# Optimization experiments

Measured on AMD Instinct MI355X. Metric: run time of the kernel, lower is better.

The kernel has to match this reference:

```python
import jax, jax.numpy as jnp
import numpy as np
import math

N_HEAD = 8
LN_EPS = 1e-5


def _layernorm(x, g, b):
    mu = jnp.mean(x, axis=-1, keepdims=True)
    var = jnp.mean(jnp.square(x - mu), axis=-1, keepdims=True)
    return (x - mu) / jnp.sqrt(var + LN_EPS) * g + b


def setup_inputs() -> dict:
    key0 = jax.random.key(0)
    ks = jax.random.split(key0, 12)
    B, L, D, E = 4, 512, 256, 5  # batch, agents, n_embd, edge_feats_dim

    def w(k, shape):
        return jax.random.normal(k, shape, dtype=jnp.float32) * 0.02

    return {
        "key": jax.random.normal(ks[0], (B, L, D), jnp.float32),
        "value": jax.random.normal(ks[1], (B, L, D), jnp.float32),
        "query": jax.random.normal(ks[2], (B, L, D), jnp.float32),
        "atten_masks": jax.random.randint(ks[3], (B, L, L), 0, 2).astype(jnp.int32),
        "edge_feats": jax.random.normal(ks[4], (B, L, L, E), jnp.float32),
        # Linear weights stored [in, out] so forward is x @ W + b
        "Wk": w(ks[5], (D, D)), "bk": jnp.zeros((D,), jnp.float32),
        "Wq": w(ks[6], (D, D)), "bq": jnp.zeros((D,), jnp.float32),
        "Wv": w(ks[7], (D, D)), "bv": jnp.zeros((D,), jnp.float32),
        "Wp": w(ks[8], (D, D)), "bp": jnp.zeros((D,), jnp.float32),
        "We1": w(ks[9], (E, D)), "be1": jnp.zeros((D,), jnp.float32),
        "ln_g": jnp.ones((D,), jnp.float32), "ln_b": jnp.zeros((D,), jnp.float32),
        "We2": w(ks[10], (D, N_HEAD)), "be2": jnp.zeros((N_HEAD,), jnp.float32),
    }


def reference(key, value, query, atten_masks, edge_feats,
              Wk, bk, Wq, bq, Wv, bv, Wp, bp,
              We1, be1, ln_g, ln_b, We2, be2):
    B, L, D = query.shape
    hd = D // N_HEAD
    # QKV projections -> [B, H, L, hd]
    q = (query @ Wq + bq).reshape(B, L, N_HEAD, hd).transpose(0, 2, 1, 3)
    k = (key @ Wk + bk).reshape(B, L, N_HEAD, hd).transpose(0, 2, 1, 3)
    v = (value @ Wv + bv).reshape(B, L, N_HEAD, hd).transpose(0, 2, 1, 3)
    # scaled attention scores [B, H, L, L]
    att = jnp.einsum('bhqd,bhkd->bhqk', q, k) * (1.0 / math.sqrt(hd))
    # edge-feature additive bias: Linear -> ReLU -> LayerNorm -> Linear(per-head)
    e = jax.nn.relu(edge_feats @ We1 + be1)          # [B, L, L, D]
    e = _layernorm(e, ln_g, ln_b)
    e = e @ We2 + be2                                # [B, L, L, H]
    att = att + e.transpose(0, 3, 1, 2)
    # additive mask (0 -> -inf), softmax over keys
    att = jnp.where(atten_masks[:, None, :, :] == 0, -jnp.inf, att)
    att = jax.nn.softmax(att, axis=-1)
    y = jnp.einsum('bhqk,bhkd->bhqd', att, v)        # [B, H, L, hd]
    y = y.transpose(0, 2, 1, 3).reshape(B, L, D)
    return y @ Wp + bp
```

## Files before the change

kernel.cpp:

```cpp
#include <hip/hip_runtime.h>
#include <hip/hip_bf16.h>

#define L_SEQ 512
#define D_EMB 256
#define NH 8
#define HD 32
#define LL (L_SEQ * L_SEQ)

typedef __attribute__((ext_vector_type(8))) short short8;
typedef __attribute__((ext_vector_type(4))) float f32x4;
typedef unsigned short ushort;

__device__ __forceinline__ float bf2f(ushort u) {
    unsigned int x = ((unsigned int)u) << 16;
    float f;
    __builtin_memcpy(&f, &x, 4);
    return f;
}
__device__ __forceinline__ ushort f2bf(float x) {
    __hip_bfloat16 h = __float2bfloat16(x);
    ushort u;
    __builtin_memcpy(&u, &h, 2);
    return u;
}
__device__ __forceinline__ unsigned int fbits(float x) {
    unsigned int u;
    __builtin_memcpy(&u, &x, 4);
    return u;
}
__device__ __forceinline__ float asf(unsigned int u) {
    float f;
    __builtin_memcpy(&f, &u, 4);
    return f;
}
__device__ __forceinline__ unsigned int cvt_pk_bf16(float a, float b) {
    unsigned int r;
    asm("v_cvt_pk_bf16_f32 %0, %1, %2" : "=v"(r) : "v"(a), "v"(b));
    return r;
}
__device__ __forceinline__ unsigned int packhi(unsigned int y, unsigned int x) {
    return __builtin_amdgcn_perm(y, x, 0x07060302u);
}
__device__ __forceinline__ uint2 cvt_hilo2(float v0, float v1) {
    unsigned int hi = cvt_pk_bf16(v0, v1);
    float h0 = asf(hi << 16);
    float h1 = asf(hi & 0xffff0000u);
    unsigned int lo = cvt_pk_bf16(v0 - h0, v1 - h1);
    uint2 r; r.x = hi; r.y = lo;
    return r;
}
__device__ __forceinline__ void gload_lds16(const float* g, float* l) {
    __builtin_amdgcn_global_load_lds(
        (const __attribute__((address_space(1))) void*)g,
        (__attribute__((address_space(3))) void*)l, 16, 0, 0);
}

__global__ __launch_bounds__(256) void prep_kernel(
    const float* __restrict__ We1, const float* __restrict__ be1,
    const float* __restrict__ g,   const float* __restrict__ bta,
    const float* __restrict__ We2, const float* __restrict__ be2,
    const float* __restrict__ Wq, const float* __restrict__ Wk,
    const float* __restrict__ Wv, const float* __restrict__ Wp,
    ushort* __restrict__ W1G, ushort* __restrict__ B2G, float* __restrict__ tail,
    ushort* __restrict__ WThi, ushort* __restrict__ WTlo)
{
    int t = threadIdx.x;
    if (blockIdx.x != 0) {
        int bx = blockIdx.x - 1;
        int w = bx >> 4, ny = bx & 15;
        const float* W = (w == 0) ? Wq : (w == 1) ? Wk : (w == 2) ? Wv : Wp;
        ushort* dh = WThi + (size_t)w * 65536;
        ushort* dl = WTlo + (size_t)w * 65536;
        int n = ny * 16 + (t >> 4);
        int k0 = (t & 15) * 16;
        ushort hbuf[16], lbuf[16];
#pragma unroll
        for (int kk = 0; kk < 16; ++kk) {
            float v = W[(size_t)(k0 + kk) * 256 + n];
            unsigned int hb = fbits(v) + 0x8000u;
            ushort hi = (ushort)(hb >> 16);
            float res = v - bf2f(hi);
            hbuf[kk] = hi;
            lbuf[kk] = (ushort)((fbits(res) + 0x8000u) >> 16);
        }
        *(short8*)(dh + (size_t)n * 256 + k0)     = *(short8*)&hbuf[0];
        *(short8*)(dh + (size_t)n * 256 + k0 + 8) = *(short8*)&hbuf[8];
        *(short8*)(dl + (size_t)n * 256 + k0)     = *(short8*)&lbuf[0];
        *(short8*)(dl + (size_t)n * 256 + k0 + 8) = *(short8*)&lbuf[8];
        return;
    }

    __shared__ float red[16][256];
    float gd = g[t], bd = bta[t];
#pragma unroll
    for (int h = 0; h < 8; ++h) {
        float w2 = We2[t * 8 + h];
        red[h][t] = gd * w2;
        red[8 + h][t] = bd * w2;
    }
    __syncthreads();
    for (int off = 128; off > 0; off >>= 1) {
        if (t < off) {
#pragma unroll
            for (int row = 0; row < 16; ++row) red[row][t] += red[row][t + off];
        }
        __syncthreads();
    }
    if (t < 8) {
        tail[t] = red[t][0];
        tail[8 + t] = red[8 + t][0] + be2[t];
    }
    if (t >= 16 && t < 32) tail[t] = 0.f;

    for (int idx = t; idx < 8192; idx += 256) {
        int j = idx & 7, lane = (idx >> 3) & 63, tile = idx >> 9;
        int m = lane & 15, q = lane >> 4;
        int k = q * 8 + j;
        int d = (m >> 2) * 64 + tile * 4 + (m & 3);
        float v = 0.f;
        bool lo = false;
        if (k < 5)        v = We1[k * 256 + d];
        else if (k < 10)  { v = We1[(k - 5) * 256 + d]; lo = true; }
        else if (k < 15)  v = We1[(k - 10) * 256 + d];
        else if (k == 15) v = be1[d];
        else if (k == 16) { v = be1[d]; lo = true; }
        ushort hi = f2bf(v);
        W1G[idx] = lo ? f2bf(v - bf2f(hi)) : hi;
    }
    for (int idx = t; idx < 4096; idx += 256) {
        int j = idx & 7, lane = (idx >> 3) & 63, kc = idx >> 9;
        int n = lane & 15, q = lane >> 4;
        int d = q * 64 + kc * 8 + j;
        ushort out;
        if (n < 8)       out = f2bf(g[d] * We2[d * 8 + n]);
        else if (n == 8) out = 0x3F80;
        else             out = 0;
        B2G[idx] = out;
    }
}

__device__ __forceinline__ void gemm_body(
    const float* __restrict__ A, const ushort* __restrict__ BH,
    const ushort* __restrict__ BL, const float* __restrict__ bias,
    float* __restrict__ C, float* __restrict__ Ct,
    int bx, int by, char* smem)
{
    ushort* Ahi = (ushort*)smem;
    ushort* Alo = (ushort*)(smem + 5120);

    int tid = threadIdx.x;
    int wv = tid >> 6, lane = tid & 63;
    int m = lane & 15, quad = lane >> 4;
    int bm = bx * 64, bn = by * 64;

    int sm = tid >> 2, sg = (tid & 3) * 8;
    const float* Arow = A + (size_t)(bm + sm) * 256 + sg;

    int nrow = bn + wv * 16 + m;
    const ushort* bhp = BH + (size_t)nrow * 256 + quad * 8;
    const ushort* blp = BL + (size_t)nrow * 256 + quad * 8;

    f32x4 acc[4];
#pragma unroll
    for (int mt = 0; mt < 4; ++mt) acc[mt] = (f32x4){0.f, 0.f, 0.f, 0.f};

    for (int k0 = 0; k0 < 256; k0 += 32) {
        float4 a0 = *(const float4*)(Arow + k0);
        float4 a1 = *(const float4*)(Arow + k0 + 4);
        uint2 c0 = cvt_hilo2(a0.x, a0.y);
        uint2 c1 = cvt_hilo2(a0.z, a0.w);
        uint2 c2 = cvt_hilo2(a1.x, a1.y);
        uint2 c3 = cvt_hilo2(a1.z, a1.w);
        if (k0) __syncthreads();
        uint4 hq; hq.x = c0.x; hq.y = c1.x; hq.z = c2.x; hq.w = c3.x;
        uint4 lq; lq.x = c0.y; lq.y = c1.y; lq.z = c2.y; lq.w = c3.y;
        *(uint4*)&Ahi[sm * 40 + sg] = hq;
        *(uint4*)&Alo[sm * 40 + sg] = lq;
        __syncthreads();

        short8 bhi = *(const short8*)(bhp + k0);
        short8 blo = *(const short8*)(blp + k0);
#pragma unroll
        for (int mt = 0; mt < 4; ++mt) {
            short8 ahi = *(const short8*)&Ahi[(mt * 16 + m) * 40 + quad * 8];
            short8 alo = *(const short8*)&Alo[(mt * 16 + m) * 40 + quad * 8];
            acc[mt] = __builtin_amdgcn_mfma_f32_16x16x32_bf16(ahi, blo, acc[mt], 0, 0, 0);
            acc[mt] = __builtin_amdgcn_mfma_f32_16x16x32_bf16(alo, bhi, acc[mt], 0, 0, 0);
            acc[mt] = __builtin_amdgcn_mfma_f32_16x16x32_bf16(ahi, bhi, acc[mt], 0, 0, 0);
        }
    }

    float bn_bias = bias[nrow];
    if (Ct) {
        int bb = bm >> 9, l0 = bm & 511;
        float* outp = Ct + ((size_t)(bb * 256 + nrow)) * 512 + l0 + quad * 4;
#pragma unroll
        for (int mt = 0; mt < 4; ++mt) {
            float4 o;
            o.x = acc[mt][0] + bn_bias; o.y = acc[mt][1] + bn_bias;
            o.z = acc[mt][2] + bn_bias; o.w = acc[mt][3] + bn_bias;
            *(float4*)(outp + mt * 16) = o;
        }
    } else {
#pragma unroll
        for (int mt = 0; mt < 4; ++mt) {
#pragma unroll
            for (int r = 0; r < 4; ++r) {
                C[(size_t)(bm + mt * 16 + quad * 4 + r) * 256 + nrow] = acc[mt][r] + bn_bias;
            }
        }
    }
}

__device__ __forceinline__ short8 make_ef8(const float4& evA, float evB, int q) {
    unsigned int hb0 = fbits(evA.x), hb1 = fbits(evA.y), hb2 = fbits(evA.z),
                 hb3 = fbits(evA.w), hb4 = fbits(evB);
    float e0 = evA.x - asf(hb0 & 0xffff0000u);
    float e1 = evA.y - asf(hb1 & 0xffff0000u);
    float e2 = evA.z - asf(hb2 & 0xffff0000u);
    float e3 = evA.w - asf(hb3 & 0xffff0000u);
    float e4 = evB   - asf(hb4 & 0xffff0000u);
    unsigned int la0 = fbits(e0) + 0x8000u;
    unsigned int la1 = fbits(e1) + 0x8000u;
    unsigned int la2 = fbits(e2) + 0x8000u;
    unsigned int la3 = fbits(e3) + 0x8000u;
    unsigned int la4 = fbits(e4) + 0x8000u;
    unsigned int A0v = packhi(hb1, hb0);
    unsigned int A1v = packhi(hb3, hb2);
    unsigned int A2v = packhi(hb0, hb4);
    unsigned int A3v = packhi(hb2, hb1);
    unsigned int B0v = packhi(hb4, hb3);
    unsigned int B1v = packhi(la1, la0);
    unsigned int B2v = packhi(la3, la2);
    unsigned int B3v = packhi(0x3F800000u, la4);
    uint4 efd;
    bool isq0 = (q == 0), isq1 = (q == 1), isq2 = (q == 2);
    efd.x = isq0 ? A0v : isq1 ? B0v : isq2 ? 0x3F80u : 0u;
    efd.y = isq0 ? A1v : isq1 ? B1v : 0u;
    efd.z = isq0 ? A2v : isq1 ? B2v : 0u;
    efd.w = isq0 ? A3v : isq1 ? B3v : 0u;
    short8 ef8;
    __builtin_memcpy(&ef8, &efd, 16);
    return ef8;
}

__device__ __forceinline__ void ln_store(
    const f32x4& acc, const f32x4& acc2, float shv, float bbv,
    int lane, int n, int q, ushort* __restrict__ E2,
    int b, int i, int jb)
{
    const float inv256 = 1.0f / 256.0f;
    int base = lane & 48;
    float er[4];
#pragma unroll
    for (int r = 0; r < 4; ++r) {
        float sm = __shfl(acc[r], base + 8);
        float sq = __shfl(acc2[r], base + (base >> 2) + r);
        float dot = acc[r];
        float mu = sm * inv256;
        float var = fmaf(-mu, mu, sq * inv256);
        float rs = rsqrtf(var + 1e-5f);
        er[r] = fmaf(dot - mu * shv, rs, bbv);
    }
    if (n < 8) {
        uint2 outv;
        outv.x = cvt_pk_bf16(er[0], er[1]);
        outv.y = cvt_pk_bf16(er[2], er[3]);
        size_t basep = (((size_t)(b * NH + n) * L_SEQ + i) * L_SEQ) + jb + q * 4;
        *(uint2*)(E2 + basep) = outv;
    }
}

__device__ __forceinline__ void edge_body(
    const float* __restrict__ EF, const ushort* __restrict__ W1G,
    const ushort* __restrict__ B2G, const float* __restrict__ tail,
    ushort* __restrict__ E2, int bi, char* smem)
{
    int tid = threadIdx.x;
    {
        const uint4* s1 = (const uint4*)W1G;
        uint4* d1 = (uint4*)smem;
#pragma unroll
        for (int k = 0; k < 4; ++k) d1[tid + k * 256] = s1[tid + k * 256];
    }
    int wv = tid >> 6, lane = tid & 63;
    int q = lane >> 4, n = lane & 15;

    short8 b2f[8];
#pragma unroll
    for (int kc = 0; kc < 8; ++kc)
        b2f[kc] = *(const short8*)(B2G + (kc * 64 + lane) * 8);

    int b = bi >> 9, i = bi & 511;
    size_t rowbase = (size_t)bi * 512;

    float shv = tail[n];
    float bbv = tail[8 + n];

    const float* efbase = EF + rowbase * 5;
    int pair0 = wv * 32 + n;

    const float* p0 = efbase + (size_t)pair0 * 5;
    float4 evA0 = *(const float4*)p0;        float evB0 = p0[4];
    float4 evA1 = *(const float4*)(p0 + 80); float evB1 = p0[84];

    __syncthreads();
    const short8* w1l = (const short8*)smem;

    const f32x4 z = {0.f, 0.f, 0.f, 0.f};

    for (int iter = 0; iter < 4; ++iter) {
        float4 nA0, nA1; float nB0 = 0.f, nB1 = 0.f;
        if (iter < 3) {
            const float* pn = efbase + (size_t)((iter + 1) * 128 + pair0) * 5;
            nA0 = *(const float4*)pn;        nB0 = pn[4];
            nA1 = *(const float4*)(pn + 80); nB1 = pn[84];
        }
        int jb0 = iter * 128 + wv * 32;

        short8 ef0 = make_ef8(evA0, evB0, q);
        short8 ef1 = make_ef8(evA1, evB1, q);

        f32x4 acc0 = z, acc20 = z, acc1 = z, acc21 = z;
#pragma unroll
        for (int kc = 0; kc < 8; ++kc) {
            short8 wa = w1l[2 * kc * 64 + lane];
            short8 wb = w1l[(2 * kc + 1) * 64 + lane];
            short8 b2 = b2f[kc];
            f32x4 dA0 = __builtin_amdgcn_mfma_f32_16x16x32_bf16(wa, ef0, z, 0, 0, 0);
            f32x4 dB0 = __builtin_amdgcn_mfma_f32_16x16x32_bf16(wb, ef0, z, 0, 0, 0);
            f32x4 dA1 = __builtin_amdgcn_mfma_f32_16x16x32_bf16(wa, ef1, z, 0, 0, 0);
            f32x4 dB1 = __builtin_amdgcn_mfma_f32_16x16x32_bf16(wb, ef1, z, 0, 0, 0);
            uint4 av0, av1;
            av0.x = cvt_pk_bf16(fmaxf(dA0[0], 0.f), fmaxf(dA0[1], 0.f));
            av0.y = cvt_pk_bf16(fmaxf(dA0[2], 0.f), fmaxf(dA0[3], 0.f));
            av0.z = cvt_pk_bf16(fmaxf(dB0[0], 0.f), fmaxf(dB0[1], 0.f));
            av0.w = cvt_pk_bf16(fmaxf(dB0[2], 0.f), fmaxf(dB0[3], 0.f));
            av1.x = cvt_pk_bf16(fmaxf(dA1[0], 0.f), fmaxf(dA1[1], 0.f));
            av1.y = cvt_pk_bf16(fmaxf(dA1[2], 0.f), fmaxf(dA1[3], 0.f));
            av1.z = cvt_pk_bf16(fmaxf(dB1[0], 0.f), fmaxf(dB1[1], 0.f));
            av1.w = cvt_pk_bf16(fmaxf(dB1[2], 0.f), fmaxf(dB1[3], 0.f));
            short8 a0, a1;
            __builtin_memcpy(&a0, &av0, 16);
            __builtin_memcpy(&a1, &av1, 16);
            acc0  = __builtin_amdgcn_mfma_f32_16x16x32_bf16(a0, b2, acc0, 0, 0, 0);
            acc20 = __builtin_amdgcn_mfma_f32_16x16x32_bf16(a0, a0, acc20, 0, 0, 0);
            acc1  = __builtin_amdgcn_mfma_f32_16x16x32_bf16(a1, b2, acc1, 0, 0, 0);
            acc21 = __builtin_amdgcn_mfma_f32_16x16x32_bf16(a1, a1, acc21, 0, 0, 0);
        }

        ln_store(acc0, acc20, shv, bbv, lane, n, q, E2, b, i, jb0);
        ln_store(acc1, acc21, shv, bbv, lane, n, q, E2, b, i, jb0 + 16);

        evA0 = nA0; evB0 = nB0;
        evA1 = nA1; evB1 = nB1;
    }
}

__global__ __launch_bounds__(256, 4) void fused_qkv_edge(
    const float* __restrict__ query, const float* __restrict__ key,
    const float* __restrict__ value,
    const ushort* __restrict__ WThi, const ushort* __restrict__ WTlo,
    const float* __restrict__ bq, const float* __restrict__ bk,
    const float* __restrict__ bv,
    float* __restrict__ Qw, float* __restrict__ Ktw, float* __restrict__ Vw,
    const float* __restrict__ EF, const ushort* __restrict__ W1G,
    const ushort* __restrict__ B2G, const float* __restrict__ tail,
    ushort* __restrict__ E2)
{
    __shared__ __align__(16) char smem[16384];
    int bid = blockIdx.x;
    if (bid < 384) {
        int z = bid >> 7, rem = bid & 127;
        int bx = rem & 31, by = rem >> 5;
        if (z == 0)
            gemm_body(query, WThi + 0 * 65536, WTlo + 0 * 65536, bq, Qw, nullptr, bx, by, smem);
        else if (z == 1)
            gemm_body(key,   WThi + 1 * 65536, WTlo + 1 * 65536, bk, nullptr, Ktw, bx, by, smem);
        else
            gemm_body(value, WThi + 2 * 65536, WTlo + 2 * 65536, bv, Vw, nullptr, bx, by, smem);
    } else {
        edge_body(EF, W1G, B2G, tail, E2, bid - 384, smem);
    }
}

__global__ __launch_bounds__(256) void gemm_out(
    const float* __restrict__ A, const ushort* __restrict__ BH,
    const ushort* __restrict__ BL, const float* __restrict__ bias,
    float* __restrict__ C)
{
    __shared__ __align__(16) char smem[10240];
    gemm_body(A, BH, BL, bias, C, nullptr, blockIdx.x, blockIdx.y, smem);
}

__global__ __launch_bounds__(256, 4) void attn_kernel(
    const float* __restrict__ Q, const float* __restrict__ Kt,
    const float* __restrict__ V, const ushort* __restrict__ E2,
    const int* __restrict__ MSK, float* __restrict__ Y)
{
    __shared__ __align__(16) float stage[2][4096];
    __shared__ ushort pbuf[4][512][4];

    int bh = blockIdx.x;
    int b = bh >> 3, h = bh & 7;
    int tid = threadIdx.x;
    int wv = tid >> 6, lane = tid & 63;
    int i0 = blockIdx.y * 16;
    int i = i0 + wv * 4;

    const float* Ktb = Kt + (size_t)bh * (HD * L_SEQ);
    const float* Vb  = V + (size_t)b * L_SEQ * D_EMB + h * HD;

    int wvu = __builtin_amdgcn_readfirstlane(wv);
    const float* Qs = Q + ((size_t)(b * L_SEQ + i0 + wvu * 4)) * 256 + h * HD;

    size_t erow = ((size_t)bh * L_SEQ + i) * L_SEQ;
    size_t mrow = ((size_t)b * L_SEQ + i) * L_SEQ;

    unsigned int e2p[4][4];
    unsigned int mkb[4];
#pragma unroll
    for (int r = 0; r < 4; ++r) {
        unsigned int mb = 0;
#pragma unroll
        for (int c = 0; c < 4; ++c) {
            int j = c * 128 + 2 * lane;
            e2p[r][c] = *(const unsigned int*)(E2 + erow + (size_t)r * L_SEQ + j);
            int2 mv = *(const int2*)(MSK + mrow + (size_t)r * L_SEQ + j);
            mb |= (mv.x != 0 ? 1u : 0u) << (2 * c);
            mb |= (mv.y != 0 ? 1u : 0u) << (2 * c + 1);
        }
        mkb[r] = mb;
    }

    float s[4][8];
#pragma unroll
    for (int r = 0; r < 4; ++r)
#pragma unroll
        for (int t = 0; t < 8; ++t) s[r][t] = 0.f;

    int kd0 = tid >> 5, ksj = (tid & 31) * 4;
#pragma unroll
    for (int p = 0; p < 4; ++p)
        gload_lds16(Ktb + (size_t)(p * 8 + kd0) * L_SEQ + ksj,
                    &stage[0][(p * 8 + kd0) * 128 + ksj]);

    for (int c = 0; c < 4; ++c) {
        __syncthreads();
        if (c < 3) {
#pragma unroll
            for (int p = 0; p < 4; ++p)
                gload_lds16(Ktb + (size_t)(p * 8 + kd0) * L_SEQ + (c + 1) * 128 + ksj,
                            &stage[(c + 1) & 1][(p * 8 + kd0) * 128 + ksj]);
        }
        const float* stg = stage[c & 1];
        int c2 = c * 2;
#pragma unroll
        for (int d = 0; d < HD; ++d) {
            float q0 = Qs[0 * 256 + d];
            float q1 = Qs[1 * 256 + d];
            float q2 = Qs[2 * 256 + d];
            float q3 = Qs[3 * 256 + d];
            float2 kv = *(const float2*)&stg[d * 128 + 2 * lane];
            s[0][c2]     = fmaf(q0, kv.x, s[0][c2]);
            s[0][c2 + 1] = fmaf(q0, kv.y, s[0][c2 + 1]);
            s[1][c2]     = fmaf(q1, kv.x, s[1][c2]);
            s[1][c2 + 1] = fmaf(q1, kv.y, s[1][c2 + 1]);
            s[2][c2]     = fmaf(q2, kv.x, s[2][c2]);
            s[2][c2 + 1] = fmaf(q2, kv.y, s[2][c2 + 1]);
            s[3][c2]     = fmaf(q3, kv.x, s[3][c2]);
            s[3][c2 + 1] = fmaf(q3, kv.y, s[3][c2 + 1]);
        }
    }

    int vj0 = tid >> 3, vdd = (tid & 7) * 4;
#pragma unroll
    for (int p = 0; p < 4; ++p)
        gload_lds16(Vb + (size_t)(p * 32 + vj0) * D_EMB + vdd,
                    &stage[0][(p * 32 + vj0) * 32 + vdd]);

    const float scl = 0.17677669529663687f;
#pragma unroll
    for (int r = 0; r < 4; ++r) {
        float m = -3.0e38f;
#pragma unroll
        for (int idx = 0; idx < 8; ++idx) {
            int c = idx >> 1, u = idx & 1;
            unsigned int pk = e2p[r][c];
            float e = bf2f((ushort)(u ? (pk >> 16) : (pk & 0xffff)));
            int mk = (mkb[r] >> idx) & 1;
            float v = mk ? fmaf(s[r][idx], scl, e) : -1e30f;
            s[r][idx] = v;
            m = fmaxf(m, v);
        }
#pragma unroll
        for (int o = 32; o > 0; o >>= 1) m = fmaxf(m, __shfl_xor(m, o));
        float ssum = 0.f;
#pragma unroll
        for (int idx = 0; idx < 8; ++idx) {
            float p = __expf(s[r][idx] - m);
            s[r][idx] = p;
            ssum += p;
        }
#pragma unroll
        for (int o = 32; o > 0; o >>= 1) ssum += __shfl_xor(ssum, o);
        float inv = 1.0f / ssum;
#pragma unroll
        for (int idx = 0; idx < 8; ++idx) s[r][idx] *= inv;
    }
#pragma unroll
    for (int c = 0; c < 4; ++c) {
        int c2 = c * 2;
        uint4 w;
        w.x = cvt_pk_bf16(s[0][c2],     s[1][c2]);
        w.y = cvt_pk_bf16(s[2][c2],     s[3][c2]);
        w.z = cvt_pk_bf16(s[0][c2 + 1], s[1][c2 + 1]);
        w.w = cvt_pk_bf16(s[2][c2 + 1], s[3][c2 + 1]);
        *(uint4*)&pbuf[wv][c * 128 + 2 * lane][0] = w;
    }

    int dg = lane >> 3, js = lane & 7;
    float4 acc[4];
#pragma unroll
    for (int r = 0; r < 4; ++r) { acc[r].x = 0.f; acc[r].y = 0.f; acc[r].z = 0.f; acc[r].w = 0.f; }

    for (int c = 0; c < 4; ++c) {
        __syncthreads();
        if (c < 3) {
#pragma unroll
            for (int p = 0; p < 4; ++p)
                gload_lds16(Vb + (size_t)((c + 1) * 128 + p * 32 + vj0) * D_EMB + vdd,
                            &stage[(c + 1) & 1][(p * 32 + vj0) * 32 + vdd]);
        }
        const float* stg = stage[c & 1];
#pragma unroll
        for (int jb = 0; jb < 16; ++jb) {
            int jj = jb * 8 + js;
            float4 v4 = *(const float4*)&stg[jj * 32 + dg * 4];
            uint2 pu = *(const uint2*)&pbuf[wv][c * 128 + jj][0];
            float p0 = asf(pu.x << 16);
            float p1 = asf(pu.x & 0xffff0000u);
            float p2 = asf(pu.y << 16);
            float p3 = asf(pu.y & 0xffff0000u);
            acc[0].x = fmaf(p0, v4.x, acc[0].x);
            acc[0].y = fmaf(p0, v4.y, acc[0].y);
            acc[0].z = fmaf(p0, v4.z, acc[0].z);
            acc[0].w = fmaf(p0, v4.w, acc[0].w);
            acc[1].x = fmaf(p1, v4.x, acc[1].x);
            acc[1].y = fmaf(p1, v4.y, acc[1].y);
            acc[1].z = fmaf(p1, v4.z, acc[1].z);
            acc[1].w = fmaf(p1, v4.w, acc[1].w);
            acc[2].x = fmaf(p2, v4.x, acc[2].x);
            acc[2].y = fmaf(p2, v4.y, acc[2].y);
            acc[2].z = fmaf(p2, v4.z, acc[2].z);
            acc[2].w = fmaf(p2, v4.w, acc[2].w);
            acc[3].x = fmaf(p3, v4.x, acc[3].x);
            acc[3].y = fmaf(p3, v4.y, acc[3].y);
            acc[3].z = fmaf(p3, v4.z, acc[3].z);
            acc[3].w = fmaf(p3, v4.w, acc[3].w);
        }
    }

#pragma unroll
    for (int off = 1; off < 8; off <<= 1) {
#pragma unroll
        for (int r = 0; r < 4; ++r) {
            acc[r].x += __shfl_xor(acc[r].x, off);
            acc[r].y += __shfl_xor(acc[r].y, off);
            acc[r].z += __shfl_xor(acc[r].z, off);
            acc[r].w += __shfl_xor(acc[r].w, off);
        }
    }
    if (js == 0) {
#pragma unroll
        for (int r = 0; r < 4; ++r)
            *(float4*)(Y + ((size_t)(b * L_SEQ + i + r)) * 256 + h * HD + dg * 4) = acc[r];
    }
}

extern "C" void kernel_launch(void* const* d_in, const int* in_sizes, int n_in,
                              void* d_out, int out_size, void* d_ws, size_t ws_size,
                              hipStream_t stream)
{
    const float* key   = (const float*)d_in[0];
    const float* value = (const float*)d_in[1];
    const float* query = (const float*)d_in[2];
    const int*   msk   = (const int*)d_in[3];
    const float* ef    = (const float*)d_in[4];
    const float* Wk  = (const float*)d_in[5];  const float* bk  = (const float*)d_in[6];
    const float* Wq  = (const float*)d_in[7];  const float* bq  = (const float*)d_in[8];
    const float* Wv  = (const float*)d_in[9];  const float* bv  = (const float*)d_in[10];
    const float* Wp  = (const float*)d_in[11]; const float* bp  = (const float*)d_in[12];
    const float* We1 = (const float*)d_in[13]; const float* be1 = (const float*)d_in[14];
    const float* lng = (const float*)d_in[15]; const float* lnb = (const float*)d_in[16];
    const float* We2 = (const float*)d_in[17]; const float* be2 = (const float*)d_in[18];

    const int MTOK = 4 * L_SEQ;
    const int NELT = MTOK * D_EMB;

    float* ws    = (float*)d_ws;
    float* Qw    = ws;
    float* Vw    = Qw + NELT;
    float* Yw    = Vw + NELT;
    float* Ktw   = Yw + NELT;
    ushort* W1G  = (ushort*)(Ktw + NELT);
    ushort* B2G  = W1G + 8192;
    float* tail  = (float*)(B2G + 4096);
    ushort* WThi = (ushort*)(tail + 32);
    ushort* WTlo = WThi + 4 * 65536;
    ushort* E2   = WTlo + 4 * 65536;

    hipLaunchKernelGGL(prep_kernel, dim3(65), dim3(256), 0, stream,
                       We1, be1, lng, lnb, We2, be2,
                       Wq, Wk, Wv, Wp,
                       W1G, B2G, tail, WThi, WTlo);
    hipLaunchKernelGGL(fused_qkv_edge, dim3(2432), dim3(256), 0, stream,
                       query, key, value, WThi, WTlo, bq, bk, bv,
                       Qw, Ktw, Vw,
                       ef, W1G, B2G, tail, E2);
    hipLaunchKernelGGL(attn_kernel, dim3(32, 32), dim3(256), 0, stream,
                       Qw, Ktw, Vw, E2, msk, Yw);
    hipLaunchKernelGGL(gemm_out, dim3(32, 4), dim3(256), 0, stream,
                       Yw, WThi + 3 * 65536, WTlo + 3 * 65536, bp, (float*)d_out);
}
```

Measured before the change: 208.8 us.

## Spread prep work over more blocks, halve output GEMM tile, stage B2G in LDS

The prep kernel now converts weights with 256 blocks of 4-element chunks and moves the W1G and B2G packing into their own blocks, so that work no longer runs serially in one block. The output projection uses a new 32-row tile GEMM, doubling its grid to give the GPU more blocks. The edge body now loads B2G fragments into shared memory instead of holding eight short8 registers per lane, cutting register pressure at the cost of 8 KB more LDS per block, which may reduce occupancy of the fused kernel.

```diff
diff --git a/kernel.cpp b/kernel.cpp
--- a/kernel.cpp
+++ b/kernel.cpp
@@ -65,17 +65,18 @@
     ushort* __restrict__ WThi, ushort* __restrict__ WTlo)
 {
     int t = threadIdx.x;
-    if (blockIdx.x != 0) {
-        int bx = blockIdx.x - 1;
-        int w = bx >> 4, ny = bx & 15;
+    int bid = blockIdx.x;
+    if (bid >= 3) {
+        int bx = bid - 3;
+        int w = bx >> 6, ny = bx & 63;
         const float* W = (w == 0) ? Wq : (w == 1) ? Wk : (w == 2) ? Wv : Wp;
         ushort* dh = WThi + (size_t)w * 65536;
         ushort* dl = WTlo + (size_t)w * 65536;
-        int n = ny * 16 + (t >> 4);
-        int k0 = (t & 15) * 16;
-        ushort hbuf[16], lbuf[16];
-#pragma unroll
-        for (int kk = 0; kk < 16; ++kk) {
+        int n = ny * 4 + (t >> 6);
+        int k0 = (t & 63) * 4;
+        ushort hbuf[4], lbuf[4];
+#pragma unroll
+        for (int kk = 0; kk < 4; ++kk) {
             float v = W[(size_t)(k0 + kk) * 256 + n];
             unsigned int hb = fbits(v) + 0x8000u;
             ushort hi = (ushort)(hb >> 16);
@@ -83,10 +84,40 @@
             hbuf[kk] = hi;
             lbuf[kk] = (ushort)((fbits(res) + 0x8000u) >> 16);
         }
-        *(short8*)(dh + (size_t)n * 256 + k0)     = *(short8*)&hbuf[0];
-        *(short8*)(dh + (size_t)n * 256 + k0 + 8) = *(short8*)&hbuf[8];
-        *(short8*)(dl + (size_t)n * 256 + k0)     = *(short8*)&lbuf[0];
-        *(short8*)(dl + (size_t)n * 256 + k0 + 8) = *(short8*)&lbuf[8];
+        *(uint2*)(dh + (size_t)n * 256 + k0) = *(uint2*)&hbuf[0];
+        *(uint2*)(dl + (size_t)n * 256 + k0) = *(uint2*)&lbuf[0];
+        return;
+    }
+
+    if (bid == 1) {
+        for (int idx = t; idx < 8192; idx += 256) {
+            int j = idx & 7, lane = (idx >> 3) & 63, tile = idx >> 9;
+            int m = lane & 15, q = lane >> 4;
+            int k = q * 8 + j;
+            int d = (m >> 2) * 64 + tile * 4 + (m & 3);
+            float v = 0.f;
+            bool lo = false;
+            if (k < 5)        v = We1[k * 256 + d];
+            else if (k < 10)  { v = We1[(k - 5) * 256 + d]; lo = true; }
+            else if (k < 15)  v = We1[(k - 10) * 256 + d];
+            else if (k == 15) v = be1[d];
+            else if (k == 16) { v = be1[d]; lo = true; }
+            ushort hi = f2bf(v);
+            W1G[idx] = lo ? f2bf(v - bf2f(hi)) : hi;
+        }
+        return;
+    }
+    if (bid == 2) {
+        for (int idx = t; idx < 4096; idx += 256) {
+            int j = idx & 7, lane = (idx >> 3) & 63, kc = idx >> 9;
+            int n = lane & 15, q = lane >> 4;
+            int d = q * 64 + kc * 8 + j;
+            ushort out;
+            if (n < 8)       out = f2bf(g[d] * We2[d * 8 + n]);
+            else if (n == 8) out = 0x3F80;
+            else             out = 0;
+            B2G[idx] = out;
+        }
         return;
     }
 
@@ -111,32 +142,6 @@
         tail[8 + t] = red[8 + t][0] + be2[t];
     }
     if (t >= 16 && t < 32) tail[t] = 0.f;
-
-    for (int idx = t; idx < 8192; idx += 256) {
-        int j = idx & 7, lane = (idx >> 3) & 63, tile = idx >> 9;
-        int m = lane & 15, q = lane >> 4;
-        int k = q * 8 + j;
-        int d = (m >> 2) * 64 + tile * 4 + (m & 3);
-        float v = 0.f;
-        bool lo = false;
-        if (k < 5)        v = We1[k * 256 + d];
-        else if (k < 10)  { v = We1[(k - 5) * 256 + d]; lo = true; }
-        else if (k < 15)  v = We1[(k - 10) * 256 + d];
-        else if (k == 15) v = be1[d];
-        else if (k == 16) { v = be1[d]; lo = true; }
-        ushort hi = f2bf(v);
-        W1G[idx] = lo ? f2bf(v - bf2f(hi)) : hi;
-    }
-    for (int idx = t; idx < 4096; idx += 256) {
-        int j = idx & 7, lane = (idx >> 3) & 63, kc = idx >> 9;
-        int n = lane & 15, q = lane >> 4;
-        int d = q * 64 + kc * 8 + j;
-        ushort out;
-        if (n < 8)       out = f2bf(g[d] * We2[d * 8 + n]);
-        else if (n == 8) out = 0x3F80;
-        else             out = 0;
-        B2G[idx] = out;
-    }
 }
 
 __device__ __forceinline__ void gemm_body(
@@ -208,6 +213,63 @@
             for (int r = 0; r < 4; ++r) {
                 C[(size_t)(bm + mt * 16 + quad * 4 + r) * 256 + nrow] = acc[mt][r] + bn_bias;
             }
+        }
+    }
+}
+
+__device__ __forceinline__ void gemm_body32(
+    const float* __restrict__ A, const ushort* __restrict__ BH,
+    const ushort* __restrict__ BL, const float* __restrict__ bias,
+    float* __restrict__ C, int bx, int by, char* smem)
+{
+    ushort* Ahi = (ushort*)smem;
+    ushort* Alo = (ushort*)(smem + 2560);
+
+    int tid = threadIdx.x;
+    int wv = tid >> 6, lane = tid & 63;
+    int m = lane & 15, quad = lane >> 4;
+    int bm = bx * 32, bn = by * 64;
+
+    int sm = tid >> 3, sg = (tid & 7) * 4;
+    const float* Arow = A + (size_t)(bm + sm) * 256 + sg;
+
+    int nrow = bn + wv * 16 + m;
+    const ushort* bhp = BH + (size_t)nrow * 256 + quad * 8;
+    const ushort* blp = BL + (size_t)nrow * 256 + quad * 8;
+
+    f32x4 acc[2];
+    acc[0] = (f32x4){0.f, 0.f, 0.f, 0.f};
+    acc[1] = (f32x4){0.f, 0.f, 0.f, 0.f};
+
+    for (int k0 = 0; k0 < 256; k0 += 32) {
+        float4 a0 = *(const float4*)(Arow + k0);
+        uint2 c0 = cvt_hilo2(a0.x, a0.y);
+        uint2 c1 = cvt_hilo2(a0.z, a0.w);
+        if (k0) __syncthreads();
+        uint2 hq; hq.x = c0.x; hq.y = c1.x;
+        uint2 lq; lq.x = c0.y; lq.y = c1.y;
+        *(uint2*)&Ahi[sm * 40 + sg] = hq;
+        *(uint2*)&Alo[sm * 40 + sg] = lq;
+        __syncthreads();
+
+        short8 bhi = *(const short8*)(bhp + k0);
+        short8 blo = *(const short8*)(blp + k0);
+#pragma unroll
+        for (int mt = 0; mt < 2; ++mt) {
+            short8 ahi = *(const short8*)&Ahi[(mt * 16 + m) * 40 + quad * 8];
+            short8 alo = *(const short8*)&Alo[(mt * 16 + m) * 40 + quad * 8];
+            acc[mt] = __builtin_amdgcn_mfma_f32_16x16x32_bf16(ahi, blo, acc[mt], 0, 0, 0);
+            acc[mt] = __builtin_amdgcn_mfma_f32_16x16x32_bf16(alo, bhi, acc[mt], 0, 0, 0);
+            acc[mt] = __builtin_amdgcn_mfma_f32_16x16x32_bf16(ahi, bhi, acc[mt], 0, 0, 0);
+        }
+    }
+
+    float bn_bias = bias[nrow];
+#pragma unroll
+    for (int mt = 0; mt < 2; ++mt) {
+#pragma unroll
+        for (int r = 0; r < 4; ++r) {
+            C[(size_t)(bm + mt * 16 + quad * 4 + r) * 256 + nrow] = acc[mt][r] + bn_bias;
         }
     }
 }
@@ -282,14 +344,13 @@
         uint4* d1 = (uint4*)smem;
 #pragma unroll
         for (int k = 0; k < 4; ++k) d1[tid + k * 256] = s1[tid + k * 256];
+        const uint4* s2 = (const uint4*)B2G;
+        uint4* d2 = (uint4*)(smem + 16384);
+#pragma unroll
+        for (int k = 0; k < 2; ++k) d2[tid + k * 256] = s2[tid + k * 256];
     }
     int wv = tid >> 6, lane = tid & 63;
     int q = lane >> 4, n = lane & 15;
-
-    short8 b2f[8];
-#pragma unroll
-    for (int kc = 0; kc < 8; ++kc)
-        b2f[kc] = *(const short8*)(B2G + (kc * 64 + lane) * 8);
 
     int b = bi >> 9, i = bi & 511;
     size_t rowbase = (size_t)bi * 512;
@@ -306,6 +367,7 @@
 
     __syncthreads();
     const short8* w1l = (const short8*)smem;
+    const short8* b2l = (const short8*)(smem + 16384);
 
     const f32x4 z = {0.f, 0.f, 0.f, 0.f};
 
@@ -326,7 +388,7 @@
         for (int kc = 0; kc < 8; ++kc) {
             short8 wa = w1l[2 * kc * 64 + lane];
             short8 wb = w1l[(2 * kc + 1) * 64 + lane];
-            short8 b2 = b2f[kc];
+            short8 b2 = b2l[kc * 64 + lane];
             f32x4 dA0 = __builtin_amdgcn_mfma_f32_16x16x32_bf16(wa, ef0, z, 0, 0, 0);
             f32x4 dB0 = __builtin_amdgcn_mfma_f32_16x16x32_bf16(wb, ef0, z, 0, 0, 0);
             f32x4 dA1 = __builtin_amdgcn_mfma_f32_16x16x32_bf16(wa, ef1, z, 0, 0, 0);
@@ -368,7 +430,7 @@
     const ushort* __restrict__ B2G, const float* __restrict__ tail,
     ushort* __restrict__ E2)
 {
-    __shared__ __align__(16) char smem[16384];
+    __shared__ __align__(16) char smem[24576];
     int bid = blockIdx.x;
     if (bid < 384) {
         int z = bid >> 7, rem = bid & 127;
@@ -389,8 +451,8 @@
     const ushort* __restrict__ BL, const float* __restrict__ bias,
     float* __restrict__ C)
 {
-    __shared__ __align__(16) char smem[10240];
-    gemm_body(A, BH, BL, bias, C, nullptr, blockIdx.x, blockIdx.y, smem);
+    __shared__ __align__(16) char smem[5120];
+    gemm_body32(A, BH, BL, bias, C, blockIdx.x, blockIdx.y, smem);
 }
 
 __global__ __launch_bounds__(256, 4) void attn_kernel(
@@ -610,7 +672,7 @@
     ushort* WTlo = WThi + 4 * 65536;
     ushort* E2   = WTlo + 4 * 65536;
 
-    hipLaunchKernelGGL(prep_kernel, dim3(65), dim3(256), 0, stream,
+    hipLaunchKernelGGL(prep_kernel, dim3(259), dim3(256), 0, stream,
                        We1, be1, lng, lnb, We2, be2,
                        Wq, Wk, Wv, Wp,
                        W1G, B2G, tail, WThi, WTlo);
@@ -620,6 +682,6 @@
                        ef, W1G, B2G, tail, E2);
     hipLaunchKernelGGL(attn_kernel, dim3(32, 32), dim3(256), 0, stream,
                        Qw, Ktw, Vw, E2, msk, Yw);
-    hipLaunchKernelGGL(gemm_out, dim3(32, 4), dim3(256), 0, stream,
+    hipLaunchKernelGGL(gemm_out, dim3(64, 4), dim3(256), 0, stream,
                        Yw, WThi + 3 * 65536, WTlo + 3 * 65536, bp, (float*)d_out);
 }
```

Result: faster. 204.4 us (-2.1%).
